# Kernel tuning notes

Measured on AMD Instinct MI355X. Metric: run time of the kernel, lower is better.

Reference implementation:

```python
import jax, jax.numpy as jnp
import numpy as np

# module hyperparameters (match init_kwargs)
C_V, C_F, C_D = 64, 128, 64
COSTS = jnp.array([4.0, 2.0, 1.0], dtype=jnp.float32)  # bandwidth cost per granularity
PENALTY = 0.0  # no_transmission_utility_penalty (min utility threshold)


def setup_inputs() -> dict:
    key = jax.random.key(0)
    k1, k2 = jax.random.split(key)
    B, H, W = 5, 256, 256
    C = C_V + C_F + C_D
    collab = jax.random.normal(k1, (B, C, H, W), dtype=jnp.float32)
    util = jax.random.normal(k2, (B, H, W, 3), dtype=jnp.float32)
    return {
        "collab_bev_data_list": collab,
        "utility_map_list": util,
        "bandwidth_budget": 150000,
    }


def _selection(utility, budget_per_sample):
    # utility: [B, H, W, G] -> selected granularity index per pixel ([B,H,W], -1.0 = not transmitted)
    B, H, W, G = utility.shape
    HW = H * W
    best_u = jnp.max(utility, axis=-1).reshape(B, HW)
    best_g = jnp.argmax(utility, axis=-1).reshape(B, HW)
    # stable descending sort by utility; ties keep row-major order (matches Python stable sort)
    order = jnp.argsort(-best_u, axis=1, stable=True)          # [B, HW]
    u_s = jnp.take_along_axis(best_u, order, axis=1)
    g_s = jnp.take_along_axis(best_g, order, axis=1)
    cost_s = COSTS[g_s]                                        # [B, HW]
    valid_s = u_s > PENALTY

    def scan_one(costs, valid):
        # sequential greedy knapsack: accept item if it still fits in the budget
        def step(usage, cv):
            c, v = cv
            accept = v & (usage + c <= budget_per_sample)
            return usage + jnp.where(accept, c, jnp.float32(0.0)), accept
        _, accepted = jax.lax.scan(step, jnp.float32(0.0), (costs, valid))
        return accepted

    accepted = jax.vmap(scan_one)(cost_s, valid_s)             # [B, HW] bool (sorted order)
    vals = jnp.where(accepted, g_s.astype(jnp.float32), -1.0)
    sel = jnp.full((B, HW), -1.0, dtype=jnp.float32)
    sel = sel.at[jnp.arange(B)[:, None], order].set(vals)      # scatter back to pixel order
    return sel.reshape(B, H, W)


def reference(collab_bev_data_list, utility_map_list, bandwidth_budget):
    cav_num = collab_bev_data_list.shape[0]
    budget_per_sample = jnp.float32(bandwidth_budget) / cav_num
    sel = _selection(utility_map_list, budget_per_sample)      # [B, H, W]
    F_vox = collab_bev_data_list[:, :C_V]
    F_feat = collab_bev_data_list[:, C_V:C_V + C_F]
    F_det = collab_bev_data_list[:, C_V + C_F:C_V + C_F + C_D]
    m = sel[:, None, :, :]                                     # [B,1,H,W]
    f_trans = jnp.concatenate([
        F_vox * (m == 0.0),
        F_feat * (m == 1.0),
        F_det * (m == 2.0),
    ], axis=1)
    return f_trans, sel
```

## Files before the change

### kernel.cpp

```cpp
#include <hip/hip_runtime.h>
#include <hip/hip_bf16.h>

#define NB 5
#define HW 65536
#define NC 256
#define LISTCAP 4096

__device__ __forceinline__ unsigned int pkey_of(float u) {
    unsigned int b = __float_as_uint(u);
    unsigned int o = (b & 0x80000000u) ? ~b : (b | 0x80000000u);
    return ~o;
}

__device__ __forceinline__ float budget_per_sample(const int* bp) {
    int v = bp[0];
    float f = (v > 0 && v < 100000000) ? (float)v : __int_as_float(v);
    return f / (float)NB;
}

__global__ void k_prep(const float* __restrict__ util,
                       unsigned int* __restrict__ pkeys,
                       unsigned char* __restrict__ meta,
                       unsigned int* __restrict__ hist) {
    int i = blockIdx.x * blockDim.x + threadIdx.x;
    if (i >= NB * HW) return;
    int b = i >> 16;
    const float* u3 = util + (size_t)i * 3;
    float u0 = u3[0], u1 = u3[1], u2 = u3[2];
    int g = 0; float u = u0;
    if (u1 > u) { u = u1; g = 1; }
    if (u2 > u) { u = u2; g = 2; }
    bool valid = u > 0.0f;
    unsigned int pk = pkey_of(u);
    pkeys[i] = pk;
    meta[i] = (unsigned char)(g | (valid ? 4 : 0));
    if (valid) {
        int cost = 4 >> g;
        atomicAdd(&hist[(b << 16) | (pk >> 16)], (unsigned int)cost);
    }
}

__global__ void __launch_bounds__(1024) k_scan(const unsigned int* __restrict__ hist,
                                               const int* __restrict__ budget_ptr,
                                               unsigned int* __restrict__ bstar,
                                               unsigned int* __restrict__ wbefore) {
    int b = blockIdx.x;
    const unsigned int* h = hist + (b << 16);
    float budget = budget_per_sample(budget_ptr);
    int t = threadIdx.x;
    unsigned int s = 0;
    #pragma unroll 4
    for (int j = 0; j < 64; ++j) s += h[t * 64 + j];
    __shared__ unsigned int ls[1024];
    ls[t] = s; __syncthreads();
    for (int off = 1; off < 1024; off <<= 1) {
        unsigned int v = (t >= off) ? ls[t - off] : 0u;
        __syncthreads();
        ls[t] += v;
        __syncthreads();
    }
    unsigned int incl = ls[t];
    unsigned int excl = incl - s;
    if ((float)excl <= budget && (float)incl > budget) {
        unsigned int cum = excl; int bb = t * 64;
        for (int j = 0; j < 64; ++j) {
            unsigned int nc = cum + h[t * 64 + j];
            if ((float)nc > budget) { bb = t * 64 + j; break; }
            cum = nc;
        }
        bstar[b] = (unsigned int)bb;
        wbefore[b] = cum;
    }
    if (t == 1023 && (float)incl <= budget) {
        bstar[b] = 65536u;
        wbefore[b] = incl;
    }
}

__global__ void k_selbase(const unsigned int* __restrict__ pkeys,
                          const unsigned char* __restrict__ meta,
                          const unsigned int* __restrict__ bstar,
                          float* __restrict__ sel,
                          char* __restrict__ sel8) {
    int i = blockIdx.x * blockDim.x + threadIdx.x;
    if (i >= NB * HW) return;
    int b = i >> 16;
    unsigned int bs = bstar[b];
    unsigned int pk = pkeys[i];
    unsigned char m = meta[i];
    bool acc = ((pk >> 16) < bs) && (m & 4);
    sel[i]  = acc ? (float)(m & 3) : -1.0f;
    sel8[i] = acc ? (char)(m & 3) : (char)-1;
}

__global__ void __launch_bounds__(1024) k_boundary(const unsigned int* __restrict__ pkeys,
                                                   const unsigned char* __restrict__ meta,
                                                   const unsigned int* __restrict__ bstar,
                                                   const unsigned int* __restrict__ wbefore,
                                                   const int* __restrict__ budget_ptr,
                                                   float* __restrict__ sel,
                                                   char* __restrict__ sel8) {
    int b = blockIdx.x;
    unsigned int bs = bstar[b];
    if (bs >= 65536u) return;
    float budget = budget_per_sample(budget_ptr);
    __shared__ unsigned long long list[LISTCAP];
    __shared__ unsigned long long red[1024];
    __shared__ unsigned int cnt;
    __shared__ float usage_sh;
    int t = threadIdx.x;
    if (t == 0) cnt = 0;
    __syncthreads();
    const unsigned int* pk_b = pkeys + (b << 16);
    const unsigned char* mt_b = meta + (b << 16);
    for (int p = t; p < HW; p += 1024) {
        unsigned int pk = pk_b[p];
        unsigned char m = mt_b[p];
        if ((pk >> 16) == bs && (m & 4)) {
            unsigned int pos = atomicAdd(&cnt, 1u);
            if (pos < LISTCAP)
                list[pos] = ((unsigned long long)pk << 32) |
                            ((unsigned long long)p << 16) | (unsigned long long)m;
        }
    }
    __syncthreads();
    int n = (int)min(cnt, (unsigned int)LISTCAP);
    int np = 1; while (np < n) np <<= 1;
    for (int i = n + t; i < np; i += 1024) list[i] = ~0ull;
    __syncthreads();
    for (int k = 2; k <= np; k <<= 1) {
        for (int j = k >> 1; j > 0; j >>= 1) {
            for (int i = t; i < np; i += 1024) {
                int ixj = i ^ j;
                if (ixj > i) {
                    unsigned long long a = list[i], c = list[ixj];
                    bool asc = ((i & k) == 0);
                    if ((a > c) == asc) { list[i] = c; list[ixj] = a; }
                }
            }
            __syncthreads();
        }
    }
    if (t == 0) {
        float usage = (float)wbefore[b];
        for (int i = 0; i < n; ++i) {
            unsigned long long v = list[i];
            int g = (int)(v & 3ull);
            float c = (float)(4 >> g);
            if (usage + c <= budget) {
                usage += c;
                int p = (int)((v >> 16) & 0xFFFFull);
                sel[(b << 16) | p]  = (float)g;
                sel8[(b << 16) | p] = (char)g;
            }
        }
        usage_sh = usage;
    }
    __syncthreads();
    float r = budget - usage_sh;
    unsigned long long lo = ((unsigned long long)(bs + 1)) << 32;
    for (int iter = 0; iter < 8; ++iter) {
        if (r < 1.0f) break;
        unsigned long long best = ~0ull;
        for (int p = t; p < HW; p += 1024) {
            unsigned char m = mt_b[p];
            if (m & 4) {
                int cost = 4 >> (m & 3);
                if ((float)cost <= r) {
                    unsigned long long c48 = ((unsigned long long)pk_b[p] << 16) |
                                             (unsigned long long)p;
                    if (c48 >= lo && c48 < best) best = c48;
                }
            }
        }
        red[t] = best; __syncthreads();
        for (int off = 512; off > 0; off >>= 1) {
            if (t < off) { if (red[t + off] < red[t]) red[t] = red[t + off]; }
            __syncthreads();
        }
        unsigned long long found = red[0];
        __syncthreads();
        if (found == ~0ull) break;
        int p = (int)(found & 0xFFFFull);
        unsigned char m = mt_b[p];
        int g = m & 3;
        if (t == 0) {
            sel[(b << 16) | p]  = (float)g;
            sel8[(b << 16) | p] = (char)g;
        }
        r -= (float)(4 >> g);
        lo = found + 1;
    }
}

__global__ void k_mask(const float4* __restrict__ in,
                       const char* __restrict__ sel8,
                       float4* __restrict__ out) {
    const unsigned int TOT4 = (unsigned int)NB * NC * (HW / 4);
    unsigned int stride = gridDim.x * blockDim.x;
    for (unsigned int i = blockIdx.x * blockDim.x + threadIdx.x; i < TOT4; i += stride) {
        unsigned int p4 = i & ((HW / 4) - 1);
        unsigned int bc = i >> 14;
        unsigned int c = bc & (NC - 1);
        unsigned int b = bc >> 8;
        int g = (c < 64) ? 0 : ((c < 192) ? 1 : 2);
        char4 s4 = *reinterpret_cast<const char4*>(sel8 + ((size_t)b << 16) + (p4 << 2));
        bool m0 = (int)s4.x == g, m1 = (int)s4.y == g,
             m2 = (int)s4.z == g, m3 = (int)s4.w == g;
        float4 v = make_float4(0.f, 0.f, 0.f, 0.f);
        if (m0 | m1 | m2 | m3) {
            float4 x = in[i];
            v.x = m0 ? x.x : 0.f;
            v.y = m1 ? x.y : 0.f;
            v.z = m2 ? x.z : 0.f;
            v.w = m3 ? x.w : 0.f;
        }
        out[i] = v;
    }
}

extern "C" void kernel_launch(void* const* d_in, const int* in_sizes, int n_in,
                              void* d_out, int out_size, void* d_ws, size_t ws_size,
                              hipStream_t stream) {
    const float* collab = (const float*)d_in[0];
    const float* util   = (const float*)d_in[1];
    const int*   budget = (const int*)d_in[2];

    float* f_trans = (float*)d_out;
    float* sel     = f_trans + (size_t)NB * NC * HW;

    char* ws = (char*)d_ws;
    unsigned int*  hist    = (unsigned int*)(ws + 0);
    unsigned int*  pkeys   = (unsigned int*)(ws + 1310720);
    unsigned char* meta    = (unsigned char*)(ws + 2621440);
    char*          sel8    = (char*)(ws + 2949120);
    unsigned int*  bstar   = (unsigned int*)(ws + 3276800);
    unsigned int*  wbefore = (unsigned int*)(ws + 3276832);

    hipMemsetAsync(hist, 0, (size_t)NB * 65536 * 4, stream);
    k_prep<<<(NB * HW + 255) / 256, 256, 0, stream>>>(util, pkeys, meta, hist);
    k_scan<<<NB, 1024, 0, stream>>>(hist, budget, bstar, wbefore);
    k_selbase<<<(NB * HW + 255) / 256, 256, 0, stream>>>(pkeys, meta, bstar, sel, sel8);
    k_boundary<<<NB, 1024, 0, stream>>>(pkeys, meta, bstar, wbefore, budget, sel, sel8);
    k_mask<<<4096, 256, 0, stream>>>((const float4*)collab, sel8, (float4*)f_trans);
}
```

Baseline: 640.9 us.

## Fuse scan, base selection and boundary kernels; restructure mask kernel per channel

```diff
diff --git a/kernel.cpp b/kernel.cpp
--- a/kernel.cpp
+++ b/kernel.cpp
@@ -1,10 +1,11 @@
 #include <hip/hip_runtime.h>
-#include <hip/hip_bf16.h>
 
 #define NB 5
 #define HW 65536
 #define NC 256
 #define LISTCAP 4096
+
+typedef float v4f __attribute__((ext_vector_type(4)));
 
 __device__ __forceinline__ unsigned int pkey_of(float u) {
     unsigned int b = __float_as_uint(u);
@@ -40,18 +41,27 @@
     }
 }
 
-__global__ void __launch_bounds__(1024) k_scan(const unsigned int* __restrict__ hist,
-                                               const int* __restrict__ budget_ptr,
-                                               unsigned int* __restrict__ bstar,
-                                               unsigned int* __restrict__ wbefore) {
+__global__ void __launch_bounds__(1024) k_select(const unsigned int* __restrict__ pkeys,
+                                                 const unsigned char* __restrict__ meta,
+                                                 const unsigned int* __restrict__ hist,
+                                                 const int* __restrict__ budget_ptr,
+                                                 float* __restrict__ sel,
+                                                 char* __restrict__ sel8) {
     int b = blockIdx.x;
+    int t = threadIdx.x;
+    float budget = budget_per_sample(budget_ptr);
+
+    __shared__ unsigned int ls[1024];
+    __shared__ unsigned int s_bstar, s_wbefore;
+    __shared__ unsigned long long list[LISTCAP];
+    __shared__ unsigned long long red[1024];
+    __shared__ unsigned int cnt;
+    __shared__ float usage_sh;
+
     const unsigned int* h = hist + (b << 16);
-    float budget = budget_per_sample(budget_ptr);
-    int t = threadIdx.x;
     unsigned int s = 0;
     #pragma unroll 4
     for (int j = 0; j < 64; ++j) s += h[t * 64 + j];
-    __shared__ unsigned int ls[1024];
     ls[t] = s; __syncthreads();
     for (int off = 1; off < 1024; off <<= 1) {
         unsigned int v = (t >= off) ? ls[t - off] : 0u;
@@ -68,62 +78,37 @@
             if ((float)nc > budget) { bb = t * 64 + j; break; }
             cum = nc;
         }
-        bstar[b] = (unsigned int)bb;
-        wbefore[b] = cum;
+        s_bstar = (unsigned int)bb;
+        s_wbefore = cum;
     }
     if (t == 1023 && (float)incl <= budget) {
-        bstar[b] = 65536u;
-        wbefore[b] = incl;
-    }
-}
-
-__global__ void k_selbase(const unsigned int* __restrict__ pkeys,
-                          const unsigned char* __restrict__ meta,
-                          const unsigned int* __restrict__ bstar,
-                          float* __restrict__ sel,
-                          char* __restrict__ sel8) {
-    int i = blockIdx.x * blockDim.x + threadIdx.x;
-    if (i >= NB * HW) return;
-    int b = i >> 16;
-    unsigned int bs = bstar[b];
-    unsigned int pk = pkeys[i];
-    unsigned char m = meta[i];
-    bool acc = ((pk >> 16) < bs) && (m & 4);
-    sel[i]  = acc ? (float)(m & 3) : -1.0f;
-    sel8[i] = acc ? (char)(m & 3) : (char)-1;
-}
-
-__global__ void __launch_bounds__(1024) k_boundary(const unsigned int* __restrict__ pkeys,
-                                                   const unsigned char* __restrict__ meta,
-                                                   const unsigned int* __restrict__ bstar,
-                                                   const unsigned int* __restrict__ wbefore,
-                                                   const int* __restrict__ budget_ptr,
-                                                   float* __restrict__ sel,
-                                                   char* __restrict__ sel8) {
-    int b = blockIdx.x;
-    unsigned int bs = bstar[b];
-    if (bs >= 65536u) return;
-    float budget = budget_per_sample(budget_ptr);
-    __shared__ unsigned long long list[LISTCAP];
-    __shared__ unsigned long long red[1024];
-    __shared__ unsigned int cnt;
-    __shared__ float usage_sh;
-    int t = threadIdx.x;
+        s_bstar = 65536u;
+        s_wbefore = incl;
+    }
     if (t == 0) cnt = 0;
     __syncthreads();
+    unsigned int bs = s_bstar;
+
     const unsigned int* pk_b = pkeys + (b << 16);
     const unsigned char* mt_b = meta + (b << 16);
+    float* sel_b = sel + (b << 16);
+    char* sel8_b = sel8 + (b << 16);
     for (int p = t; p < HW; p += 1024) {
         unsigned int pk = pk_b[p];
         unsigned char m = mt_b[p];
-        if ((pk >> 16) == bs && (m & 4)) {
+        bool acc = ((pk >> 16) < bs) && (m & 4);
+        sel_b[p]  = acc ? (float)(m & 3) : -1.0f;
+        sel8_b[p] = acc ? (char)(m & 3) : (char)-1;
+        if (acc == false && (pk >> 16) == bs && (m & 4)) {
             unsigned int pos = atomicAdd(&cnt, 1u);
             if (pos < LISTCAP)
                 list[pos] = ((unsigned long long)pk << 32) |
                             ((unsigned long long)p << 16) | (unsigned long long)m;
         }
     }
-    __syncthreads();
+    if (bs >= 65536u) return;
+    __syncthreads();
+
     int n = (int)min(cnt, (unsigned int)LISTCAP);
     int np = 1; while (np < n) np <<= 1;
     for (int i = n + t; i < np; i += 1024) list[i] = ~0ull;
@@ -141,8 +126,9 @@
             __syncthreads();
         }
     }
+
     if (t == 0) {
-        float usage = (float)wbefore[b];
+        float usage = (float)s_wbefore;
         for (int i = 0; i < n; ++i) {
             unsigned long long v = list[i];
             int g = (int)(v & 3ull);
@@ -150,13 +136,14 @@
             if (usage + c <= budget) {
                 usage += c;
                 int p = (int)((v >> 16) & 0xFFFFull);
-                sel[(b << 16) | p]  = (float)g;
-                sel8[(b << 16) | p] = (char)g;
+                sel_b[p]  = (float)g;
+                sel8_b[p] = (char)g;
             }
         }
         usage_sh = usage;
     }
     __syncthreads();
+
     float r = budget - usage_sh;
     unsigned long long lo = ((unsigned long long)(bs + 1)) << 32;
     for (int iter = 0; iter < 8; ++iter) {
@@ -185,37 +172,39 @@
         unsigned char m = mt_b[p];
         int g = m & 3;
         if (t == 0) {
-            sel[(b << 16) | p]  = (float)g;
-            sel8[(b << 16) | p] = (char)g;
+            sel_b[p]  = (float)g;
+            sel8_b[p] = (char)g;
         }
         r -= (float)(4 >> g);
         lo = found + 1;
     }
 }
 
-__global__ void k_mask(const float4* __restrict__ in,
-                       const char* __restrict__ sel8,
-                       float4* __restrict__ out) {
-    const unsigned int TOT4 = (unsigned int)NB * NC * (HW / 4);
-    unsigned int stride = gridDim.x * blockDim.x;
-    for (unsigned int i = blockIdx.x * blockDim.x + threadIdx.x; i < TOT4; i += stride) {
-        unsigned int p4 = i & ((HW / 4) - 1);
-        unsigned int bc = i >> 14;
-        unsigned int c = bc & (NC - 1);
-        unsigned int b = bc >> 8;
-        int g = (c < 64) ? 0 : ((c < 192) ? 1 : 2);
-        char4 s4 = *reinterpret_cast<const char4*>(sel8 + ((size_t)b << 16) + (p4 << 2));
-        bool m0 = (int)s4.x == g, m1 = (int)s4.y == g,
-             m2 = (int)s4.z == g, m3 = (int)s4.w == g;
-        float4 v = make_float4(0.f, 0.f, 0.f, 0.f);
+__global__ void __launch_bounds__(256) k_mask(const v4f* __restrict__ in,
+                                              const unsigned int* __restrict__ sel32,
+                                              v4f* __restrict__ out) {
+    int bc = blockIdx.x;
+    int b  = bc >> 8;
+    int c  = bc & 255;
+    unsigned int g = (c < 64) ? 0u : ((c < 192) ? 1u : 2u);
+    const unsigned int* sp = sel32 + (b << 14);
+    const v4f* ip = in  + (size_t)bc * (HW / 4);
+    v4f*       op = out + (size_t)bc * (HW / 4);
+    for (int p4 = threadIdx.x; p4 < HW / 4; p4 += 256) {
+        unsigned int s = sp[p4];
+        bool m0 = ((s        & 0xffu) == g);
+        bool m1 = (((s >> 8) & 0xffu) == g);
+        bool m2 = (((s >> 16)& 0xffu) == g);
+        bool m3 = ((s >> 24)          == g);
+        v4f v = {0.f, 0.f, 0.f, 0.f};
         if (m0 | m1 | m2 | m3) {
-            float4 x = in[i];
+            v4f x = __builtin_nontemporal_load(ip + p4);
             v.x = m0 ? x.x : 0.f;
             v.y = m1 ? x.y : 0.f;
             v.z = m2 ? x.z : 0.f;
             v.w = m3 ? x.w : 0.f;
         }
-        out[i] = v;
+        __builtin_nontemporal_store(v, op + p4);
     }
 }
 
@@ -230,17 +219,14 @@
     float* sel     = f_trans + (size_t)NB * NC * HW;
 
     char* ws = (char*)d_ws;
-    unsigned int*  hist    = (unsigned int*)(ws + 0);
-    unsigned int*  pkeys   = (unsigned int*)(ws + 1310720);
-    unsigned char* meta    = (unsigned char*)(ws + 2621440);
-    char*          sel8    = (char*)(ws + 2949120);
-    unsigned int*  bstar   = (unsigned int*)(ws + 3276800);
-    unsigned int*  wbefore = (unsigned int*)(ws + 3276832);
+    unsigned int*  hist  = (unsigned int*)(ws + 0);
+    unsigned int*  pkeys = (unsigned int*)(ws + 1310720);
+    unsigned char* meta  = (unsigned char*)(ws + 2621440);
+    char*          sel8  = (char*)(ws + 2949120);
 
     hipMemsetAsync(hist, 0, (size_t)NB * 65536 * 4, stream);
     k_prep<<<(NB * HW + 255) / 256, 256, 0, stream>>>(util, pkeys, meta, hist);
-    k_scan<<<NB, 1024, 0, stream>>>(hist, budget, bstar, wbefore);
-    k_selbase<<<(NB * HW + 255) / 256, 256, 0, stream>>>(pkeys, meta, bstar, sel, sel8);
-    k_boundary<<<NB, 1024, 0, stream>>>(pkeys, meta, bstar, wbefore, budget, sel, sel8);
-    k_mask<<<4096, 256, 0, stream>>>((const float4*)collab, sel8, (float4*)f_trans);
-}
+    k_select<<<NB, 1024, 0, stream>>>(pkeys, meta, hist, budget, sel, sel8);
+    k_mask<<<NB * NC, 256, 0, stream>>>((const v4f*)collab,
+                                        (const unsigned int*)sel8, (v4f*)f_trans);
+}
```

New measurement: 639.4 us. Within noise of the previous version (-0.2%).
